# Optimization experiments

Hardware: AMD Instinct MI355X
Metric: run time of the kernel (lower is better)

## Reference

```python
import jax, jax.numpy as jnp
import numpy as np

B, N, D, H = 64, 257, 1024, 16
HD = D // H  # 64


def setup_inputs() -> dict:
    key = jax.random.key(0)
    k1, k2, k3, k4, k5, k6 = jax.random.split(key, 6)
    x = jax.random.normal(k1, (B, N, D), dtype=jnp.float32)
    # boolean key mask per batch; never mask CLS token (col 0) so no fully-masked rows
    mask = jax.random.randint(k2, (B, N), 0, 2) > 0
    mask = mask.at[:, 0].set(False)
    s = 1.0 / np.sqrt(D)
    in_proj_w = jax.random.normal(k3, (3 * D, D), dtype=jnp.float32) * s
    in_proj_b = jax.random.normal(k4, (3 * D,), dtype=jnp.float32) * 0.02
    out_proj_w = jax.random.normal(k5, (D, D), dtype=jnp.float32) * s
    out_proj_b = jax.random.normal(k6, (D,), dtype=jnp.float32) * 0.02
    return {"x": x, "mask": mask, "in_proj_w": in_proj_w, "in_proj_b": in_proj_b,
            "out_proj_w": out_proj_w, "out_proj_b": out_proj_b}


def reference(x, mask, in_proj_w, in_proj_b, out_proj_w, out_proj_b):
    b, n, d = x.shape
    h, hd = H, d // H
    # fused QKV projection: [b, n, 3*d]
    qkv = jnp.einsum('bnd,ed->bne', x, in_proj_w) + in_proj_b
    # einops 'b n (qkv h d) -> qkv b h n d'
    qkv = qkv.reshape(b, n, 3, h, hd).transpose(2, 0, 3, 1, 4)
    q, k, v = qkv[0], qkv[1], qkv[2]  # each [b, h, n, hd]
    attn_weights = jnp.einsum('bhqe,bhke->bhqk', q, k) / jnp.sqrt(jnp.asarray(hd, x.dtype))
    # mode == 'mask': -inf on masked keys (broadcast over heads and queries)
    attn_weights = jnp.where(mask[:, None, None, :], -jnp.inf, attn_weights)
    attn_matrix = jax.nn.softmax(attn_weights, axis=-1)
    out = jnp.einsum('bhqk,bhke->bhqe', attn_matrix, v)  # [b, h, n, hd]
    out = out.transpose(0, 2, 1, 3).reshape(b, n, d)      # 'b h n d -> b n (h d)'
    return jnp.einsum('bnd,ed->bne', out, out_proj_w) + out_proj_b
```

## Files before the change

### kernel.cpp

```cpp
#include <hip/hip_runtime.h>

#define B_   64
#define N_   257
#define D_   1024
#define H_   16
#define HD_  64
#define M_   (B_*N_)
#define CK_  96
#define VTS_ 128
#define PLS_ 104

typedef __bf16 bf16x8 __attribute__((ext_vector_type(8)));
typedef __bf16 bf16x4 __attribute__((ext_vector_type(4)));
typedef float  f32x4  __attribute__((ext_vector_type(4)));

__device__ __forceinline__ void gload_lds16(const void* g, void* l) {
    __builtin_amdgcn_global_load_lds(
        (const __attribute__((address_space(1))) void*)g,
        (__attribute__((address_space(3))) void*)l, 16, 0, 0);
}

__global__ __launch_bounds__(256) void cvt_f32_bf16(const float* __restrict__ src,
                                                    __bf16* __restrict__ dst, int n4) {
    int i = blockIdx.x * 256 + threadIdx.x;
    if (i >= n4) return;
    float4 v = reinterpret_cast<const float4*>(src)[i];
    bf16x4 o;
    o[0] = (__bf16)v.x; o[1] = (__bf16)v.y; o[2] = (__bf16)v.z; o[3] = (__bf16)v.w;
    *reinterpret_cast<bf16x4*>(dst + (size_t)i * 4) = o;
}

__global__ __launch_bounds__(256) void qkv_gemm(const __bf16* __restrict__ A,
                                                const __bf16* __restrict__ W,
                                                const float* __restrict__ bias,
                                                __bf16* __restrict__ qw,
                                                __bf16* __restrict__ kw,
                                                __bf16* __restrict__ vw) {
    __shared__ __align__(16) char smem[32768];
    __bf16* As = (__bf16*)smem;
    __bf16* Ws = (__bf16*)(smem + 16384);
    __bf16* Ct = (__bf16*)smem;
    const int tid  = threadIdx.x;
    const int row0 = blockIdx.x * 128, col0 = blockIdx.y * 128;
    const int lane = tid & 63, wv = tid >> 6;
    const int wm = (wv >> 1) * 64, wn = (wv & 1) * 64;
    const int fr = lane & 15, fq = lane >> 4;
    size_t sA[4], sW[4];
#pragma unroll
    for (int i = 0; i < 4; ++i) {
        const int c = tid + i * 256;
        const int r = c >> 3, g = (c & 7) ^ (r & 7);
        sA[i] = (size_t)(row0 + r) * 1024 + g * 8;
        sW[i] = (size_t)(col0 + r) * 1024 + g * 8;
    }
    const int fsw = ((fr & 7)) * 8;
    f32x4 acc[4][4] = {};
    for (int k0 = 0; k0 < 1024; k0 += 64) {
#pragma unroll
        for (int i = 0; i < 4; ++i) {
            gload_lds16(A + sA[i] + k0, (char*)As + i * 4096 + wv * 1024);
            gload_lds16(W + sW[i] + k0, (char*)Ws + i * 4096 + wv * 1024);
        }
        __syncthreads();
#pragma unroll
        for (int ks = 0; ks < 2; ++ks) {
            const int goff = (((ks * 4 + fq) ^ (fr & 7)) * 8);
            bf16x8 af[4], bw[4];
#pragma unroll
            for (int i = 0; i < 4; ++i)
                af[i] = *reinterpret_cast<const bf16x8*>(&As[(wm + i * 16 + fr) * 64 + goff]);
#pragma unroll
            for (int j = 0; j < 4; ++j)
                bw[j] = *reinterpret_cast<const bf16x8*>(&Ws[(wn + j * 16 + fr) * 64 + goff]);
#pragma unroll
            for (int i = 0; i < 4; ++i)
#pragma unroll
                for (int j = 0; j < 4; ++j)
                    acc[i][j] = __builtin_amdgcn_mfma_f32_16x16x32_bf16(af[i], bw[j], acc[i][j], 0, 0, 0);
        }
        __syncthreads();
    }
    const int which = col0 >> 10;
    __bf16* dst = which == 0 ? qw : (which == 1 ? kw : vw);
    const float scale = which == 0 ? 0.125f : 1.0f;
    float bj[4];
#pragma unroll
    for (int j = 0; j < 4; ++j) bj[j] = bias[col0 + wn + j * 16 + fr];
#pragma unroll
    for (int i = 0; i < 4; ++i)
#pragma unroll
        for (int r = 0; r < 4; ++r) {
            const int row = wm + i * 16 + fq * 4 + r;
#pragma unroll
            for (int j = 0; j < 4; ++j)
                Ct[row * 128 + wn + j * 16 + fr] = (__bf16)((acc[i][j][r] + bj[j]) * scale);
        }
    __syncthreads();
    const int h0 = (col0 >> 6) & 15;
    const int col = (tid & 15) * 8;
    const int h = h0 + (col >> 6), hd = col & 63;
#pragma unroll
    for (int p = 0; p < 8; ++p) {
        const int row = p * 16 + (tid >> 4);
        const int m = row0 + row;
        if (m < M_) {
            bf16x8 v = *reinterpret_cast<const bf16x8*>(&Ct[row * 128 + col]);
            const int bb = m / 257, nn = m - bb * 257;
            *reinterpret_cast<bf16x8*>(dst + ((size_t)(bb * 16 + h) * 257 + nn) * 64 + hd) = v;
        }
    }
}

__global__ __launch_bounds__(256) void attn_kernel(const __bf16* __restrict__ qw,
                                                   const __bf16* __restrict__ kw,
                                                   const __bf16* __restrict__ vw,
                                                   const int* __restrict__ mask,
                                                   __bf16* __restrict__ attn) {
    const int bh = blockIdx.x;
    const int bb = bh >> 4, hh = bh & 15;
    const int q0 = blockIdx.y * 64;
    const int tid = threadIdx.x, lane = tid & 63, wv = tid >> 6;
    const int fr = lane & 15, fq = lane >> 4;
    const float NEG_INF = -__builtin_inff();

    __shared__ __align__(16) __bf16 Qs[64 * 64];
    __shared__ __align__(16) __bf16 Ks[CK_ * 64];
    __shared__ __align__(16) __bf16 Vt[64 * VTS_];
    __shared__ __align__(16) __bf16 Pl[4][16 * PLS_];
    __shared__ float maskb[288];

    const __bf16* qg = qw + ((size_t)bh * 257 + q0) * 64;
    const __bf16* kg = kw + (size_t)bh * 257 * 64;
    const __bf16* vg = vw + (size_t)bh * 257 * 64;
    const int* mg = mask + bb * 257;

    for (int idx = tid; idx < 288; idx += 256)
        maskb[idx] = (idx < 257 && mg[idx] == 0) ? 0.0f : NEG_INF;

#pragma unroll
    for (int i = 0; i < 2; ++i) {
        const int c = tid + i * 256;
        const int r = c >> 3, g = (c & 7) ^ (r & 7);
        if (q0 + r < 257)
            gload_lds16(qg + (size_t)r * 64 + g * 8, (char*)Qs + i * 4096 + wv * 1024);
    }

    float m_run[4] = {NEG_INF, NEG_INF, NEG_INF, NEG_INF};
    float l_run[4] = {};
    f32x4 Oa[4] = {};

    for (int c3 = 0; c3 < 3; ++c3) {
        const int k0 = c3 * CK_;
        __syncthreads();
#pragma unroll
        for (int i = 0; i < 3; ++i) {
            const int c = tid + i * 256;
            const int r = c >> 3, g = (c & 7) ^ (r & 7);
            if (k0 + r < 257)
                gload_lds16(kg + (size_t)(k0 + r) * 64 + g * 8, (char*)Ks + i * 4096 + wv * 1024);
        }
#pragma unroll
        for (int it = 0; it < 3; ++it) {
            const int t = tid + it * 256;
            const int key = t >> 3, grp = t & 7;
            if (k0 + key < 257) {
                bf16x8 v8 = *reinterpret_cast<const bf16x8*>(vg + (size_t)(k0 + key) * 64 + grp * 8);
#pragma unroll
                for (int u = 0; u < 8; ++u) {
                    const int hd = grp * 8 + u;
                    Vt[hd * VTS_ + (((key >> 3) ^ (hd & 7)) * 8) + (key & 7)] = v8[u];
                }
            }
        }
        __syncthreads();

        f32x4 s[6];
        {
            bf16x8 aq[2];
#pragma unroll
            for (int ks = 0; ks < 2; ++ks)
                aq[ks] = *reinterpret_cast<const bf16x8*>(
                    &Qs[(wv * 16 + fr) * 64 + (((ks * 4 + fq) ^ (fr & 7)) * 8)]);
#pragma unroll
            for (int nt = 0; nt < 6; ++nt) {
                f32x4 sa = {};
#pragma unroll
                for (int ks = 0; ks < 2; ++ks) {
                    bf16x8 bk = *reinterpret_cast<const bf16x8*>(
                        &Ks[(nt * 16 + fr) * 64 + (((ks * 4 + fq) ^ (fr & 7)) * 8)]);
                    sa = __builtin_amdgcn_mfma_f32_16x16x32_bf16(aq[ks], bk, sa, 0, 0, 0);
                }
                const float mb = maskb[k0 + nt * 16 + fr];
#pragma unroll
                for (int r = 0; r < 4; ++r) sa[r] += mb;
                s[nt] = sa;
            }
        }
        float alpha[4];
#pragma unroll
        for (int r = 0; r < 4; ++r) {
            float v = s[0][r];
#pragma unroll
            for (int nt = 1; nt < 6; ++nt) v = fmaxf(v, s[nt][r]);
            v = fmaxf(v, __shfl_xor(v, 1));
            v = fmaxf(v, __shfl_xor(v, 2));
            v = fmaxf(v, __shfl_xor(v, 4));
            v = fmaxf(v, __shfl_xor(v, 8));
            const float mnew = fmaxf(m_run[r], v);
            alpha[r] = __expf(m_run[r] - mnew);
            m_run[r] = mnew;
        }
        float sm[4] = {};
#pragma unroll
        for (int nt = 0; nt < 6; ++nt)
#pragma unroll
            for (int r = 0; r < 4; ++r) {
                const float p = __expf(s[nt][r] - m_run[r]);
                s[nt][r] = p;
                sm[r] += p;
            }
#pragma unroll
        for (int r = 0; r < 4; ++r) {
            float v = sm[r];
            v += __shfl_xor(v, 1);
            v += __shfl_xor(v, 2);
            v += __shfl_xor(v, 4);
            v += __shfl_xor(v, 8);
            l_run[r] = l_run[r] * alpha[r] + v;
        }
#pragma unroll
        for (int ot = 0; ot < 4; ++ot)
#pragma unroll
            for (int r = 0; r < 4; ++r) Oa[ot][r] *= alpha[r];
#pragma unroll
        for (int nt = 0; nt < 6; ++nt)
#pragma unroll
            for (int r = 0; r < 4; ++r)
                Pl[wv][(fq * 4 + r) * PLS_ + nt * 16 + fr] = (__bf16)s[nt][r];
        __syncthreads();
        bf16x8 ap[3];
#pragma unroll
        for (int kk = 0; kk < 3; ++kk)
            ap[kk] = *reinterpret_cast<const bf16x8*>(&Pl[wv][fr * PLS_ + kk * 32 + fq * 8]);
#pragma unroll
        for (int ot = 0; ot < 4; ++ot) {
            const int row = ot * 16 + fr;
#pragma unroll
            for (int kk = 0; kk < 3; ++kk) {
                bf16x8 bv = *reinterpret_cast<const bf16x8*>(
                    &Vt[row * VTS_ + (((kk * 4 + fq) ^ (fr & 7)) * 8)]);
                Oa[ot] = __builtin_amdgcn_mfma_f32_16x16x32_bf16(ap[kk], bv, Oa[ot], 0, 0, 0);
            }
        }
    }
#pragma unroll
    for (int r = 0; r < 4; ++r) {
        const int n = q0 + wv * 16 + fq * 4 + r;
        if (n < 257) {
            const float inv = 1.0f / l_run[r];
#pragma unroll
            for (int ot = 0; ot < 4; ++ot)
                attn[((size_t)(bb * 257 + n)) * 1024 + hh * 64 + ot * 16 + fr] =
                    (__bf16)(Oa[ot][r] * inv);
        }
    }
}

__global__ __launch_bounds__(256) void out_gemm(const __bf16* __restrict__ A,
                                                const __bf16* __restrict__ W,
                                                const float* __restrict__ bias,
                                                float* __restrict__ out) {
    __shared__ __align__(16) char smem[32768];
    __bf16* As = (__bf16*)smem;
    __bf16* Ws = (__bf16*)(smem + 16384);
    const int tid  = threadIdx.x;
    const int row0 = blockIdx.x * 128, col0 = blockIdx.y * 128;
    const int lane = tid & 63, wv = tid >> 6;
    const int wm = (wv >> 1) * 64, wn = (wv & 1) * 64;
    const int fr = lane & 15, fq = lane >> 4;
    size_t sA[4], sW[4];
#pragma unroll
    for (int i = 0; i < 4; ++i) {
        const int c = tid + i * 256;
        const int r = c >> 3, g = (c & 7) ^ (r & 7);
        sA[i] = (size_t)(row0 + r) * 1024 + g * 8;
        sW[i] = (size_t)(col0 + r) * 1024 + g * 8;
    }
    f32x4 acc[4][4] = {};
    for (int k0 = 0; k0 < 1024; k0 += 64) {
#pragma unroll
        for (int i = 0; i < 4; ++i) {
            gload_lds16(A + sA[i] + k0, (char*)As + i * 4096 + wv * 1024);
            gload_lds16(W + sW[i] + k0, (char*)Ws + i * 4096 + wv * 1024);
        }
        __syncthreads();
#pragma unroll
        for (int ks = 0; ks < 2; ++ks) {
            const int goff = (((ks * 4 + fq) ^ (fr & 7)) * 8);
            bf16x8 af[4], bw[4];
#pragma unroll
            for (int i = 0; i < 4; ++i)
                af[i] = *reinterpret_cast<const bf16x8*>(&As[(wm + i * 16 + fr) * 64 + goff]);
#pragma unroll
            for (int j = 0; j < 4; ++j)
                bw[j] = *reinterpret_cast<const bf16x8*>(&Ws[(wn + j * 16 + fr) * 64 + goff]);
#pragma unroll
            for (int i = 0; i < 4; ++i)
#pragma unroll
                for (int j = 0; j < 4; ++j)
                    acc[i][j] = __builtin_amdgcn_mfma_f32_16x16x32_bf16(af[i], bw[j], acc[i][j], 0, 0, 0);
        }
        __syncthreads();
    }
    float bj[4];
#pragma unroll
    for (int j = 0; j < 4; ++j) bj[j] = bias[col0 + wn + j * 16 + fr];
#pragma unroll
    for (int i = 0; i < 4; ++i)
#pragma unroll
        for (int r = 0; r < 4; ++r) {
            const int m = row0 + wm + i * 16 + fq * 4 + r;
            if (m < M_) {
                float* p = out + (size_t)m * 1024 + col0 + wn + fr;
#pragma unroll
                for (int j = 0; j < 4; ++j) p[j * 16] = acc[i][j][r] + bj[j];
            }
        }
}

extern "C" void kernel_launch(void* const* d_in, const int* in_sizes, int n_in,
                              void* d_out, int out_size, void* d_ws, size_t ws_size,
                              hipStream_t stream) {
    const float* x  = (const float*)d_in[0];
    const int* mask = (const int*)d_in[1];
    const float* w1 = (const float*)d_in[2];
    const float* b1 = (const float*)d_in[3];
    const float* w2 = (const float*)d_in[4];
    const float* b2 = (const float*)d_in[5];
    float* out = (float*)d_out;
    char* ws = (char*)d_ws;
    __bf16* x_bf  = (__bf16*)(ws);
    __bf16* w1_bf = (__bf16*)(ws + 33816576);
    __bf16* w2_bf = (__bf16*)(ws + 40108032);
    __bf16* q_ws  = (__bf16*)(ws + 42205184);
    __bf16* k_ws  = (__bf16*)(ws + 75890688);
    __bf16* v_ws  = (__bf16*)(ws + 109576192);
    __bf16* a_bf  = (__bf16*)(ws + 143261696);

    cvt_f32_bf16<<<16448, 256, 0, stream>>>(x, x_bf, 4210688);
    cvt_f32_bf16<<<3072, 256, 0, stream>>>(w1, w1_bf, 786432);
    cvt_f32_bf16<<<1024, 256, 0, stream>>>(w2, w2_bf, 262144);
    qkv_gemm<<<dim3(129, 24), 256, 0, stream>>>(x_bf, w1_bf, b1, q_ws, k_ws, v_ws);
    attn_kernel<<<dim3(1024, 5), 256, 0, stream>>>(q_ws, k_ws, v_ws, mask, a_bf);
    out_gemm<<<dim3(129, 8), 256, 0, stream>>>(a_bf, w2_bf, b2, out);
}
```

Measured before the change: 468.4 us.

## Merge conversions, remap GEMM tiles per XCD, split attention tail rows

Merges the three fp32-to-bf16 conversion launches into one kernel. Both GEMMs now use a 1D grid that remaps block IDs so blocks sharing an XCD cover contiguous row tiles, which should improve L2 reuse, and the partial last row tile is handled by trailing blocks. The attention kernel now covers only the first 256 queries, so the bounds checks in its inner path go away. A small new kernel computes the single leftover query row per (batch, head) with scalar math, at the cost of one extra launch.

```diff
diff --git a/kernel.cpp b/kernel.cpp
--- a/kernel.cpp
+++ b/kernel.cpp
@@ -20,14 +20,25 @@
         (__attribute__((address_space(3))) void*)l, 16, 0, 0);
 }
 
-__global__ __launch_bounds__(256) void cvt_f32_bf16(const float* __restrict__ src,
-                                                    __bf16* __restrict__ dst, int n4) {
+#define XQ_  4210688
+#define W1Q_ 786432
+#define W2Q_ 262144
+__global__ __launch_bounds__(256) void cvt_all(const float* __restrict__ x,
+                                               const float* __restrict__ w1,
+                                               const float* __restrict__ w2,
+                                               __bf16* __restrict__ xb,
+                                               __bf16* __restrict__ w1b,
+                                               __bf16* __restrict__ w2b) {
     int i = blockIdx.x * 256 + threadIdx.x;
-    if (i >= n4) return;
-    float4 v = reinterpret_cast<const float4*>(src)[i];
+    const float* src; __bf16* dst; int j;
+    if (i < XQ_) { src = x; dst = xb; j = i; }
+    else if (i < XQ_ + W1Q_) { src = w1; dst = w1b; j = i - XQ_; }
+    else if (i < XQ_ + W1Q_ + W2Q_) { src = w2; dst = w2b; j = i - XQ_ - W1Q_; }
+    else return;
+    float4 v = reinterpret_cast<const float4*>(src)[j];
     bf16x4 o;
     o[0] = (__bf16)v.x; o[1] = (__bf16)v.y; o[2] = (__bf16)v.z; o[3] = (__bf16)v.w;
-    *reinterpret_cast<bf16x4*>(dst + (size_t)i * 4) = o;
+    *reinterpret_cast<bf16x4*>(dst + (size_t)j * 4) = o;
 }
 
 __global__ __launch_bounds__(256) void qkv_gemm(const __bf16* __restrict__ A,
@@ -40,8 +51,17 @@
     __bf16* As = (__bf16*)smem;
     __bf16* Ws = (__bf16*)(smem + 16384);
     __bf16* Ct = (__bf16*)smem;
+    const int bid = blockIdx.x;
+    int rowt, colt;
+    if (bid < 3072) {
+        const int xcd = bid & 7, idx = bid >> 3;
+        colt = idx >> 4;
+        rowt = xcd * 16 + (idx & 15);
+    } else {
+        rowt = 128; colt = bid - 3072;
+    }
+    const int row0 = rowt * 128, col0 = colt * 128;
     const int tid  = threadIdx.x;
-    const int row0 = blockIdx.x * 128, col0 = blockIdx.y * 128;
     const int lane = tid & 63, wv = tid >> 6;
     const int wm = (wv >> 1) * 64, wn = (wv & 1) * 64;
     const int fr = lane & 15, fq = lane >> 4;
@@ -53,7 +73,6 @@
         sA[i] = (size_t)(row0 + r) * 1024 + g * 8;
         sW[i] = (size_t)(col0 + r) * 1024 + g * 8;
     }
-    const int fsw = ((fr & 7)) * 8;
     f32x4 acc[4][4] = {};
     for (int k0 = 0; k0 < 1024; k0 += 64) {
 #pragma unroll
@@ -141,8 +160,7 @@
     for (int i = 0; i < 2; ++i) {
         const int c = tid + i * 256;
         const int r = c >> 3, g = (c & 7) ^ (r & 7);
-        if (q0 + r < 257)
-            gload_lds16(qg + (size_t)r * 64 + g * 8, (char*)Qs + i * 4096 + wv * 1024);
+        gload_lds16(qg + (size_t)r * 64 + g * 8, (char*)Qs + i * 4096 + wv * 1024);
     }
 
     float m_run[4] = {NEG_INF, NEG_INF, NEG_INF, NEG_INF};
@@ -256,13 +274,72 @@
 #pragma unroll
     for (int r = 0; r < 4; ++r) {
         const int n = q0 + wv * 16 + fq * 4 + r;
-        if (n < 257) {
-            const float inv = 1.0f / l_run[r];
-#pragma unroll
-            for (int ot = 0; ot < 4; ++ot)
-                attn[((size_t)(bb * 257 + n)) * 1024 + hh * 64 + ot * 16 + fr] =
-                    (__bf16)(Oa[ot][r] * inv);
-        }
+        const float inv = 1.0f / l_run[r];
+#pragma unroll
+        for (int ot = 0; ot < 4; ++ot)
+            attn[((size_t)(bb * 257 + n)) * 1024 + hh * 64 + ot * 16 + fr] =
+                (__bf16)(Oa[ot][r] * inv);
+    }
+}
+
+__global__ __launch_bounds__(320) void attn_tail(const __bf16* __restrict__ qw,
+                                                 const __bf16* __restrict__ kw,
+                                                 const __bf16* __restrict__ vw,
+                                                 const int* __restrict__ mask,
+                                                 __bf16* __restrict__ attn) {
+    const int bh = blockIdx.x;
+    const int bb = bh >> 4, hh = bh & 15;
+    const int tid = threadIdx.x, wv = tid >> 6;
+    const float NEG_INF = -__builtin_inff();
+    __shared__ float pbuf[257];
+    __shared__ float red[5];
+    __shared__ float gstat[2];
+
+    const __bf16* qg = qw + ((size_t)bh * 257 + 256) * 64;
+    const __bf16* kg = kw + (size_t)bh * 257 * 64;
+    const __bf16* vg = vw + (size_t)bh * 257 * 64;
+
+    float s = NEG_INF;
+    if (tid < 257) {
+        const __bf16* kr = kg + (size_t)tid * 64;
+        float acc = 0.0f;
+#pragma unroll
+        for (int g = 0; g < 8; ++g) {
+            bf16x8 qv = *reinterpret_cast<const bf16x8*>(qg + g * 8);
+            bf16x8 kv = *reinterpret_cast<const bf16x8*>(kr + g * 8);
+#pragma unroll
+            for (int u = 0; u < 8; ++u) acc += (float)qv[u] * (float)kv[u];
+        }
+        s = (mask[bb * 257 + tid] == 0) ? acc : NEG_INF;
+    }
+    float v = s;
+#pragma unroll
+    for (int d = 1; d < 64; d <<= 1) v = fmaxf(v, __shfl_xor(v, d));
+    if ((tid & 63) == 0) red[wv] = v;
+    __syncthreads();
+    if (tid == 0) {
+        float m = red[0];
+#pragma unroll
+        for (int w = 1; w < 5; ++w) m = fmaxf(m, red[w]);
+        gstat[0] = m;
+    }
+    __syncthreads();
+    const float gmax = gstat[0];
+    float p = (tid < 257) ? __expf(s - gmax) : 0.0f;
+    if (tid < 257) pbuf[tid] = p;
+    float sv = p;
+#pragma unroll
+    for (int d = 1; d < 64; d <<= 1) sv += __shfl_xor(sv, d);
+    if ((tid & 63) == 0) red[wv] = sv;
+    __syncthreads();
+    if (tid == 0) gstat[1] = red[0] + red[1] + red[2] + red[3] + red[4];
+    __syncthreads();
+    if (tid < 64) {
+        const float inv = 1.0f / gstat[1];
+        float o = 0.0f;
+        for (int j = 0; j < 257; ++j)
+            o += pbuf[j] * (float)vg[(size_t)j * 64 + tid];
+        attn[((size_t)(bb * 257 + 256)) * 1024 + hh * 64 + tid] = (__bf16)(o * inv);
     }
 }
 
@@ -273,8 +350,17 @@
     __shared__ __align__(16) char smem[32768];
     __bf16* As = (__bf16*)smem;
     __bf16* Ws = (__bf16*)(smem + 16384);
+    const int bid = blockIdx.x;
+    int rowt, colt;
+    if (bid < 1024) {
+        const int xcd = bid & 7, idx = bid >> 3;
+        colt = idx >> 4;
+        rowt = xcd * 16 + (idx & 15);
+    } else {
+        rowt = 128; colt = bid - 1024;
+    }
+    const int row0 = rowt * 128, col0 = colt * 128;
     const int tid  = threadIdx.x;
-    const int row0 = blockIdx.x * 128, col0 = blockIdx.y * 128;
     const int lane = tid & 63, wv = tid >> 6;
     const int wm = (wv >> 1) * 64, wn = (wv & 1) * 64;
     const int fr = lane & 15, fq = lane >> 4;
@@ -347,10 +433,9 @@
     __bf16* v_ws  = (__bf16*)(ws + 109576192);
     __bf16* a_bf  = (__bf16*)(ws + 143261696);
 
-    cvt_f32_bf16<<<16448, 256, 0, stream>>>(x, x_bf, 4210688);
-    cvt_f32_bf16<<<3072, 256, 0, stream>>>(w1, w1_bf, 786432);
-    cvt_f32_bf16<<<1024, 256, 0, stream>>>(w2, w2_bf, 262144);
-    qkv_gemm<<<dim3(129, 24), 256, 0, stream>>>(x_bf, w1_bf, b1, q_ws, k_ws, v_ws);
-    attn_kernel<<<dim3(1024, 5), 256, 0, stream>>>(q_ws, k_ws, v_ws, mask, a_bf);
-    out_gemm<<<dim3(129, 8), 256, 0, stream>>>(a_bf, w2_bf, b2, out);
-}
+    cvt_all<<<20544, 256, 0, stream>>>(x, w1, w2, x_bf, w1_bf, w2_bf);
+    qkv_gemm<<<3096, 256, 0, stream>>>(x_bf, w1_bf, b1, q_ws, k_ws, v_ws);
+    attn_kernel<<<dim3(1024, 4), 256, 0, stream>>>(q_ws, k_ws, v_ws, mask, a_bf);
+    attn_tail<<<1024, 320, 0, stream>>>(q_ws, k_ws, v_ws, mask, a_bf);
+    out_gemm<<<1032, 256, 0, stream>>>(a_bf, w2_bf, b2, out);
+}
```

Result: faster. 452.7 us (-3.3%).
